# Optimization experiments

Hardware: AMD Instinct MI355X
Metric: run time of the kernel (lower is better)

Reference implementation:

```python
import jax, jax.numpy as jnp
import numpy as np

# hypercfg constants (init_kwargs)
AUX = 0.05
L1W = 5.0
VPW = 1.0
VNW = 1.0


def _lsa_square(cost):
    """Jonker-Volgenant shortest-augmenting-path Hungarian on a square numpy
    cost matrix. Returns rows[j] = row assigned to column j. Runs on host,
    mirroring the original CPU scipy.optimize.linear_sum_assignment call."""
    n = cost.shape[0]
    INF = np.inf
    u = np.zeros(n + 1)
    v = np.zeros(n + 1)
    p = np.zeros(n + 1, dtype=np.int64)   # p[j] = row matched to column j (1-indexed)
    way = np.zeros(n + 1, dtype=np.int64)
    for i in range(1, n + 1):
        p[0] = i
        j0 = 0
        minv = np.full(n + 1, INF)
        used = np.zeros(n + 1, dtype=bool)
        while True:
            used[j0] = True
            i0 = p[j0]
            cur = cost[i0 - 1, :] - u[i0] - v[1:]
            free = ~used[1:]
            upd = free & (cur < minv[1:])
            minv1 = minv[1:]
            minv1[upd] = cur[upd]
            way1 = way[1:]
            way1[upd] = j0
            mfree = np.where(free, minv1, INF)
            j1 = int(np.argmin(mfree)) + 1
            delta = mfree[j1 - 1]
            used_idx = np.nonzero(used)[0]
            u[p[used_idx]] += delta
            v[used_idx] -= delta
            minv1[free] -= delta
            j0 = j1
            if p[j0] == 0:
                break
        while j0 != 0:
            j1 = way[j0]
            p[j0] = p[j1]
            j0 = j1
    return p[1:] - 1


def _match(cost_mk):
    """Rectangular assignment, cost [M, K] with K <= M: pad with a constant
    column block (dummy columns cost the same for any row, so the real K
    columns get the optimal assignment, matching scipy on rectangles)."""
    M, K = cost_mk.shape
    pad = np.zeros((M, M), dtype=np.float64)
    pad[:, :K] = cost_mk
    rows = _lsa_square(pad)
    return rows[:K]


def _cost(meta_points, meta_visibles, gtpoints, gtvisibles):
    # meta_points: [S,B,L,M,2]  gtpoints: [S,B,K,2]
    # meta_visibles: [S,B,M,1]  gtvisibles: [S,B,K,1]
    S, B, L, M, _ = meta_points.shape
    # pairwise L1 cost: [S,B,L,M,K]
    diff = jnp.abs(meta_points[:, :, :, :, None, :] - gtpoints[:, :, None, None, :, :]).sum(-1)
    # delta[l] = L - (l+1), per-layer slack (torch.linspace(1, L, L))
    delta = (L - jnp.arange(1, L + 1, dtype=meta_points.dtype)) * AUX
    cost_p_ml = jax.nn.relu(diff - delta[None, None, :, None, None])
    gtv = gtvisibles[:, :, :, 0][:, :, None, :]          # [S,B,1,K]
    cost_p = gtv * cost_p_ml.mean(2)                     # [S,B,M,K]
    cost_vp = -gtv * jnp.log(meta_visibles)              # [S,B,M,1] -> [S,B,M,K]
    cost_vn = -(1.0 - gtv) * jnp.log(1.0 - meta_visibles)
    cost = L1W * cost_p + VPW * cost_vp + VNW * cost_vn  # [S,B,M,K]
    return cost.mean(0)                                  # mean over shots -> [B,M,K]


def setup_inputs() -> dict:
    key = jax.random.key(0)
    ks = jax.random.split(key, 5)
    S, B, L, M, K = 6, 16, 8, 256, 128
    meta_points = jax.random.uniform(ks[0], (S, B, L, M, 2), dtype=jnp.float32)
    # keep probabilities strictly inside (0,1) so log() is finite
    meta_visibles = jax.random.uniform(ks[1], (S, B, M, 1), dtype=jnp.float32) * 0.9 + 0.05
    covisibles = jax.random.uniform(ks[2], (B, K), dtype=jnp.float32)
    gtpoints = jax.random.uniform(ks[3], (S, B, K, 2), dtype=jnp.float32)
    gtvisibles = (jax.random.uniform(ks[4], (S, B, K, 1)) > 0.5).astype(jnp.float32)
    return {
        "meta_points": meta_points,
        "meta_visibles": meta_visibles,
        "covisibles": covisibles,
        "gtpoints": gtpoints,
        "gtvisibles": gtvisibles,
    }


def reference(meta_points, meta_visibles, covisibles, gtpoints, gtvisibles):
    # covisibles only provides the batch size in the original module
    cost = np.asarray(jax.jit(_cost)(meta_points, meta_visibles, gtpoints, gtvisibles))
    bs = cost.shape[0]
    # per-batch Hungarian on host (sequential data-dependent algorithm);
    # result[b, k] = meta index matched to keypoint k (already kp-sorted,
    # matching the argsort-reorder in the torch code)
    out = np.stack([_match(cost[b]) for b in range(bs)])
    return jnp.asarray(out, dtype=jnp.int64)
```

## Files before the change

### kernel.cpp

```cpp
#include <hip/hip_runtime.h>
#include <math.h>


#define S_ 6
#define B_ 16
#define L_ 8
#define M_ 256
#define K_ 128

__global__ void cost_kernel(const float* __restrict__ mp,
                            const float* __restrict__ mv,
                            const float* __restrict__ gt,
                            const float* __restrict__ gv,
                            float* __restrict__ cost)
{
#pragma clang fp contract(off)
    const int b = blockIdx.x;
    const int m = blockIdx.y;
    const int k = threadIdx.x;

    float accS = 0.0f;
    for (int s = 0; s < S_; ++s) {
        const int sb = s * B_ + b;
        const float gx = gt[(sb * K_ + k) * 2 + 0];
        const float gy = gt[(sb * K_ + k) * 2 + 1];
        float accL = 0.0f;
#pragma unroll
        for (int l = 0; l < L_; ++l) {
            const int base = ((sb * L_ + l) * M_ + m) * 2;
            const float dx = fabsf(mp[base + 0] - gx);
            const float dy = fabsf(mp[base + 1] - gy);
            const float diff = dx + dy;
            const float dl = (float)(L_ - (l + 1)) * 0.05f;
            const float t = diff - dl;
            accL += fmaxf(t, 0.0f);
        }
        const float meanL = accL * 0.125f;
        const float mvv = mv[sb * M_ + m];
        const float gtv = gv[sb * K_ + k];
        const float lp = -logf(mvv);
        const float ln = -logf(1.0f - mvv);
        const float val = (gtv != 0.0f) ? (5.0f * meanL + lp) : ln;
        accS += val;
    }
    cost[(b * M_ + m) * K_ + k] = accS * (1.0f / 6.0f);
}

__device__ __forceinline__ double bits2d(int lo, int hi) {
    const unsigned long long u =
        ((unsigned long long)(unsigned)hi << 32) | (unsigned)lo;
    return __longlong_as_double((long long)u);
}
__device__ __forceinline__ void d2bits(double d, int& lo, int& hi) {
    const unsigned long long u = (unsigned long long)__double_as_longlong(d);
    lo = (int)(u & 0xffffffffull);
    hi = (int)(u >> 32);
}

__global__ __launch_bounds__(64, 1) void match_kernel(const float* __restrict__ cost,
                                                      int* __restrict__ out)
{
#pragma clang fp contract(off)
    const int b = blockIdx.x;
    const int lane = threadIdx.x;
    const float* C = cost + (size_t)b * M_ * K_;
    const double INF = __builtin_inf();
    const int BIG = 0x7fffffff;

    __shared__ float  C_lds[M_ * K_];
    __shared__ double u_lds[257];
    __shared__ int    p_lds[257];

    for (int t = lane; t < (M_ * K_) / 4; t += 64)
        ((float4*)C_lds)[t] = ((const float4*)C)[t];

    for (int t = lane; t < 257; t += 64) {
        u_lds[t] = 0.0;
        p_lds[t] = (t >= 129) ? (t - 128) : 0;
    }
    __syncthreads();

    double v0 = 0.0, v1 = 0.0, v2 = 0.0, v3 = 0.0;

    for (int i = 129; i <= 256; ++i) {
        int used = 0;
        const int pj0 = p_lds[2 * lane + 1];
        const int pj1 = p_lds[2 * lane + 2];
        const int pj2 = p_lds[2 * lane + 129];
        const int pj3 = p_lds[2 * lane + 130];
        double ur0 = u_lds[pj0], ur1 = u_lds[pj1];
        double ur2 = u_lds[pj2], ur3 = u_lds[pj3];
        const double up0 = ur0, up1 = ur1, up2 = ur2, up3 = ur3;

        float2 cc = *(const float2*)(C_lds + (i - 1) * K_ + 2 * lane);
        double u_i0 = 0.0;
        int j1 = 0;
        double usum = 0.0;

        for (;;) {
            double cd0 = ((double)cc.x - u_i0) - v0;
            double cd1 = ((double)cc.y - u_i0) - v1;
            double cd2 = (0.0 - u_i0) - v2;
            double cd3 = (0.0 - u_i0) - v3;
            if (used & 1) cd0 = INF;
            if (used & 2) cd1 = INF;
            if (used & 4) cd2 = INF;
            if (used & 8) cd3 = INF;

            const double m01 = fmin(cd0, cd1);
            const double m23 = fmin(cd2, cd3);
            double bv = fmin(m01, m23);

            int lo, hi; d2bits(bv, lo, hi);
#define MIN_STAGE(CTRL, RM)                                                      \
            {                                                                    \
                const int nlo = __builtin_amdgcn_update_dpp(lo, lo, CTRL, RM, 0xf, false); \
                const int nhi = __builtin_amdgcn_update_dpp(hi, hi, CTRL, RM, 0xf, false); \
                const double mv2 = fmin(bits2d(lo, hi), bits2d(nlo, nhi));       \
                d2bits(mv2, lo, hi);                                             \
            }
            MIN_STAGE(0x111, 0xf)
            MIN_STAGE(0x112, 0xf)
            MIN_STAGE(0x114, 0xf)
            MIN_STAGE(0x118, 0xf)
            MIN_STAGE(0x142, 0xa)
            MIN_STAGE(0x143, 0xc)
#undef MIN_STAGE
            const int mlo = __builtin_amdgcn_readlane(lo, 63);
            const int mhi = __builtin_amdgcn_readlane(hi, 63);
            const double delta = bits2d(mlo, mhi);

            int jr = BIG;
            if (cd1 == delta) jr = 2 * lane + 2;
            if (cd0 == delta) jr = 2 * lane + 1;
            int jd = BIG;
            if (cd3 == delta) jd = 2 * lane + 130;
            if (cd2 == delta) jd = 2 * lane + 129;
            const unsigned long long br = __ballot(jr != BIG);
            const unsigned long long bd = __ballot(jd != BIG);
            const unsigned long long bb = br ? br : bd;
            const int cand = (br != 0ull) ? jr : jd;
            j1 = __builtin_amdgcn_readlane(cand, (int)__builtin_ctzll(bb));

            int ol, sl;
            if (j1 >= 129) { ol = (j1 - 129) >> 1; sl = 2 + ((j1 - 129) & 1); }
            else           { ol = (j1 - 1) >> 1;   sl = (j1 - 1) & 1; }
            const int psel = (sl == 0) ? pj0 : (sl == 1) ? pj1 : (sl == 2) ? pj2 : pj3;
            const int i0n = (j1 >= 129) ? (j1 - 128)
                                        : __builtin_amdgcn_readlane(psel, ol);

            const int rown = (i0n > 0 ? i0n : 1) - 1;
            const float2 ccn = *(const float2*)(C_lds + rown * K_ + 2 * lane);

            usum += delta;
            if (used & 1) { ur0 += delta; v0 -= delta; }
            if (used & 2) { ur1 += delta; v1 -= delta; }
            if (used & 4) { ur2 += delta; v2 -= delta; }
            if (used & 8) { ur3 += delta; v3 -= delta; }

            const double usel = (sl == 0) ? up0 : (sl == 1) ? up1 : (sl == 2) ? up2 : up3;
            int ulo, uhi; d2bits(usel, ulo, uhi);
            const double u_n = bits2d(__builtin_amdgcn_readlane(ulo, ol),
                                      __builtin_amdgcn_readlane(uhi, ol));

            if (i0n == 0) break;

            if (lane == ol) used |= (1 << sl);
            u_i0 = u_n;
            cc = ccn;
        }

        __syncthreads();
        if (used & 1) u_lds[pj0] = ur0;
        if (used & 2) u_lds[pj1] = ur1;
        if (used & 4) u_lds[pj2] = ur2;
        if (used & 8) u_lds[pj3] = ur3;
        if (lane == 0) { p_lds[j1] = i; u_lds[i] = usum; }
        __syncthreads();
    }

    for (int j = lane; j < K_; j += 64)
        out[b * K_ + j] = p_lds[j + 1] - 1;
}

extern "C" void kernel_launch(void* const* d_in, const int* in_sizes, int n_in,
                              void* d_out, int out_size, void* d_ws, size_t ws_size,
                              hipStream_t stream) {
    const float* mp = (const float*)d_in[0];
    const float* mv = (const float*)d_in[1];
    const float* gt = (const float*)d_in[3];
    const float* gv = (const float*)d_in[4];
    int* out = (int*)d_out;
    float* cost = (float*)d_ws;

    dim3 gridA(B_, M_);
    cost_kernel<<<gridA, K_, 0, stream>>>(mp, mv, gt, gv, cost);
    match_kernel<<<B_, 64, 0, stream>>>(cost, out);
}
```

Before: 1.417 ms.

## Handle dummy columns via per-row sorted queue instead of scanning them

Result: slower. 1.558 ms (+9.9%).

```diff
diff --git a/kernel.cpp b/kernel.cpp
--- a/kernel.cpp
+++ b/kernel.cpp
@@ -56,6 +56,13 @@
     lo = (int)(u & 0xffffffffull);
     hi = (int)(u >> 32);
 }
+__device__ __forceinline__ unsigned long long vkey_desc(double v) {
+    const double c = v + 0.0;
+    const unsigned long long bts = (unsigned long long)__double_as_longlong(c);
+    const unsigned long long mask =
+        (unsigned long long)((long long)bts >> 63) | 0x8000000000000000ull;
+    return ~(bts ^ mask);
+}
 
 __global__ __launch_bounds__(64, 1) void match_kernel(const float* __restrict__ cost,
                                                       int* __restrict__ out)
@@ -67,9 +74,13 @@
     const double INF = __builtin_inf();
     const int BIG = 0x7fffffff;
 
-    __shared__ float  C_lds[M_ * K_];
-    __shared__ double u_lds[257];
-    __shared__ int    p_lds[257];
+    __shared__ float   C_lds[M_ * K_];
+    __shared__ double  u_lds[257];
+    __shared__ int     p_lds[257];
+    __shared__ double  vd_lds[128];
+    __shared__ double2 vurec[130];
+    __shared__ int     jrec[130];
+    __shared__ double  Dcons[128];
 
     for (int t = lane; t < (M_ * K_) / 4; t += 64)
         ((float4*)C_lds)[t] = ((const float4*)C)[t];
@@ -78,38 +89,72 @@
         u_lds[t] = 0.0;
         p_lds[t] = (t >= 129) ? (t - 128) : 0;
     }
+    for (int t = lane; t < 128; t += 64) vd_lds[t] = 0.0;
     __syncthreads();
 
-    double v0 = 0.0, v1 = 0.0, v2 = 0.0, v3 = 0.0;
+    double v0 = 0.0, v1 = 0.0;
 
     for (int i = 129; i <= 256; ++i) {
-        int used = 0;
         const int pj0 = p_lds[2 * lane + 1];
         const int pj1 = p_lds[2 * lane + 2];
-        const int pj2 = p_lds[2 * lane + 129];
-        const int pj3 = p_lds[2 * lane + 130];
-        double ur0 = u_lds[pj0], ur1 = u_lds[pj1];
-        double ur2 = u_lds[pj2], ur3 = u_lds[pj3];
-        const double up0 = ur0, up1 = ur1, up2 = ur2, up3 = ur3;
-
         float2 cc = *(const float2*)(C_lds + (i - 1) * K_ + 2 * lane);
+        const double up0 = u_lds[pj0], up1 = u_lds[pj1];
+        double ur0 = up0, ur1 = up1;
+
+        unsigned long long ks0 = vkey_desc(vd_lds[2 * lane]);
+        unsigned long long ks1 = vkey_desc(vd_lds[2 * lane + 1]);
+        int js0 = 2 * lane + 129;
+        int js1 = 2 * lane + 130;
+        for (int k = 2; k <= 128; k <<= 1) {
+            const bool asc = ((lane & (k >> 1)) == 0);
+            for (int d2 = k >> 1; d2 >= 1; d2 >>= 1) {
+                if (d2 == 1) {
+                    const bool L = (ks0 < ks1) || (ks0 == ks1 && js0 < js1);
+                    if (L != asc) {
+                        const unsigned long long tk = ks0; ks0 = ks1; ks1 = tk;
+                        const int tj = js0; js0 = js1; js1 = tj;
+                    }
+                } else {
+                    const int d = d2 >> 1;
+                    const unsigned long long pk0 = __shfl_xor(ks0, d);
+                    const int pj0s = __shfl_xor(js0, d);
+                    const unsigned long long pk1 = __shfl_xor(ks1, d);
+                    const int pj1s = __shfl_xor(js1, d);
+                    const bool lower = ((lane & d) == 0);
+                    const bool L0 = (ks0 < pk0) || (ks0 == pk0 && js0 < pj0s);
+                    const bool L1 = (ks1 < pk1) || (ks1 == pk1 && js1 < pj1s);
+                    const bool keep0 = (lower == asc) ? L0 : !L0;
+                    const bool keep1 = (lower == asc) ? L1 : !L1;
+                    if (!keep0) { ks0 = pk0; js0 = pj0s; }
+                    if (!keep1) { ks1 = pk1; js1 = pj1s; }
+                }
+            }
+        }
+        jrec[2 * lane] = js0;
+        jrec[2 * lane + 1] = js1;
+        vurec[2 * lane]     = make_double2(vd_lds[js0 - 129], u_lds[js0 - 128]);
+        vurec[2 * lane + 1] = make_double2(vd_lds[js1 - 129], u_lds[js1 - 128]);
+        if (lane == 0) { vurec[128] = make_double2(-INF, 0.0); jrec[128] = 257; }
+        __syncthreads();
+
+        double2 vuC = vurec[0]; int jdC = jrec[0];
+        double2 vuN = vurec[1]; int jdN = jrec[1];
+        int ptr = 0;
+
+        int used = 0;
         double u_i0 = 0.0;
+        double usum = 0.0;
         int j1 = 0;
-        double usum = 0.0;
 
         for (;;) {
+            const float2 ccs = *(const float2*)(C_lds + (jdC - 129) * K_ + 2 * lane);
+            const double dval = (0.0 - u_i0) - vuC.x;
+
             double cd0 = ((double)cc.x - u_i0) - v0;
             double cd1 = ((double)cc.y - u_i0) - v1;
-            double cd2 = (0.0 - u_i0) - v2;
-            double cd3 = (0.0 - u_i0) - v3;
             if (used & 1) cd0 = INF;
             if (used & 2) cd1 = INF;
-            if (used & 4) cd2 = INF;
-            if (used & 8) cd3 = INF;
-
-            const double m01 = fmin(cd0, cd1);
-            const double m23 = fmin(cd2, cd3);
-            double bv = fmin(m01, m23);
+            double bv = fmin(cd0, cd1);
 
             int lo, hi; d2bits(bv, lo, hi);
 #define MIN_STAGE(CTRL, RM)                                                      \
@@ -128,53 +173,62 @@
 #undef MIN_STAGE
             const int mlo = __builtin_amdgcn_readlane(lo, 63);
             const int mhi = __builtin_amdgcn_readlane(hi, 63);
-            const double delta = bits2d(mlo, mhi);
-
-            int jr = BIG;
-            if (cd1 == delta) jr = 2 * lane + 2;
-            if (cd0 == delta) jr = 2 * lane + 1;
-            int jd = BIG;
-            if (cd3 == delta) jd = 2 * lane + 130;
-            if (cd2 == delta) jd = 2 * lane + 129;
-            const unsigned long long br = __ballot(jr != BIG);
-            const unsigned long long bd = __ballot(jd != BIG);
-            const unsigned long long bb = br ? br : bd;
-            const int cand = (br != 0ull) ? jr : jd;
-            j1 = __builtin_amdgcn_readlane(cand, (int)__builtin_ctzll(bb));
-
-            int ol, sl;
-            if (j1 >= 129) { ol = (j1 - 129) >> 1; sl = 2 + ((j1 - 129) & 1); }
-            else           { ol = (j1 - 1) >> 1;   sl = (j1 - 1) & 1; }
-            const int psel = (sl == 0) ? pj0 : (sl == 1) ? pj1 : (sl == 2) ? pj2 : pj3;
-            const int i0n = (j1 >= 129) ? (j1 - 128)
-                                        : __builtin_amdgcn_readlane(psel, ol);
-
-            const int rown = (i0n > 0 ? i0n : 1) - 1;
-            const float2 ccn = *(const float2*)(C_lds + rown * K_ + 2 * lane);
-
-            usum += delta;
-            if (used & 1) { ur0 += delta; v0 -= delta; }
-            if (used & 2) { ur1 += delta; v1 -= delta; }
-            if (used & 4) { ur2 += delta; v2 -= delta; }
-            if (used & 8) { ur3 += delta; v3 -= delta; }
-
-            const double usel = (sl == 0) ? up0 : (sl == 1) ? up1 : (sl == 2) ? up2 : up3;
-            int ulo, uhi; d2bits(usel, ulo, uhi);
-            const double u_n = bits2d(__builtin_amdgcn_readlane(ulo, ol),
-                                      __builtin_amdgcn_readlane(uhi, ol));
-
-            if (i0n == 0) break;
-
-            if (lane == ol) used |= (1 << sl);
-            u_i0 = u_n;
-            cc = ccn;
+            const double rmin = bits2d(mlo, mhi);
+
+            if (rmin <= dval) {
+                const double delta = rmin;
+                usum += delta;
+                if (used & 1) { ur0 += delta; v0 -= delta; }
+                if (used & 2) { ur1 += delta; v1 -= delta; }
+
+                int jr = BIG;
+                if (cd1 == delta) jr = 2 * lane + 2;
+                if (cd0 == delta) jr = 2 * lane + 1;
+                const unsigned long long br = __ballot(jr != BIG);
+                j1 = __builtin_amdgcn_readlane(jr, (int)__builtin_ctzll(br));
+
+                const int ol = (j1 - 1) >> 1, sl = (j1 - 1) & 1;
+                const int psel = sl ? pj1 : pj0;
+                const int i0n = __builtin_amdgcn_readlane(psel, ol);
+                if (i0n == 0) break;
+
+                const double usel = sl ? up1 : up0;
+                int ulo, uhi; d2bits(usel, ulo, uhi);
+                const double u_n = bits2d(__builtin_amdgcn_readlane(ulo, ol),
+                                          __builtin_amdgcn_readlane(uhi, ol));
+                if (lane == ol) used |= (1 << sl);
+                u_i0 = u_n;
+                cc = *(const float2*)(C_lds + (i0n - 1) * K_ + 2 * lane);
+            } else {
+                const double delta = dval;
+                usum += delta;
+                if (used & 1) { ur0 += delta; v0 -= delta; }
+                if (used & 2) { ur1 += delta; v1 -= delta; }
+                if (lane == 0) Dcons[ptr] = usum;
+                u_i0 = vuC.y;
+                cc = ccs;
+                vuC = vuN; jdC = jdN;
+                ++ptr;
+                vuN = vurec[ptr + 1]; jdN = jrec[ptr + 1];
+            }
         }
 
         __syncthreads();
         if (used & 1) u_lds[pj0] = ur0;
         if (used & 2) u_lds[pj1] = ur1;
-        if (used & 4) u_lds[pj2] = ur2;
-        if (used & 8) u_lds[pj3] = ur3;
+        {
+            const int t0i = 2 * lane, t1i = 2 * lane + 1;
+            if (t0i < ptr) {
+                const double amt = usum - Dcons[t0i];
+                u_lds[js0 - 128] += amt;
+                vd_lds[js0 - 129] -= amt;
+            }
+            if (t1i < ptr) {
+                const double amt = usum - Dcons[t1i];
+                u_lds[js1 - 128] += amt;
+                vd_lds[js1 - 129] -= amt;
+            }
+        }
         if (lane == 0) { p_lds[j1] = i; u_lds[i] = usum; }
         __syncthreads();
     }
```

## Track dummy-column minimum via precomputed max-v candidate in Hungarian loop

Applied to the files above, without the earlier changes.

Result: slower. 1.485 ms (+4.8%).

```diff
diff --git a/kernel.cpp b/kernel.cpp
--- a/kernel.cpp
+++ b/kernel.cpp
@@ -56,6 +56,26 @@
     lo = (int)(u & 0xffffffffull);
     hi = (int)(u >> 32);
 }
+__device__ __forceinline__ double readlane_d(double d, int l) {
+    int lo, hi; d2bits(d, lo, hi);
+    return bits2d(__builtin_amdgcn_readlane(lo, l),
+                  __builtin_amdgcn_readlane(hi, l));
+}
+
+#define RSTG(LOV, HIV, FOP, CTRL, RM)                                            \
+    {                                                                            \
+        const int nlo_ = __builtin_amdgcn_update_dpp(LOV, LOV, CTRL, RM, 0xf, false); \
+        const int nhi_ = __builtin_amdgcn_update_dpp(HIV, HIV, CTRL, RM, 0xf, false); \
+        const double r_ = FOP(bits2d(LOV, HIV), bits2d(nlo_, nhi_));             \
+        d2bits(r_, LOV, HIV);                                                    \
+    }
+#define RLADDER(LOV, HIV, FOP)                                                   \
+    RSTG(LOV, HIV, FOP, 0x111, 0xf)                              \
+    RSTG(LOV, HIV, FOP, 0x112, 0xf)                              \
+    RSTG(LOV, HIV, FOP, 0x114, 0xf)                              \
+    RSTG(LOV, HIV, FOP, 0x118, 0xf)                              \
+    RSTG(LOV, HIV, FOP, 0x142, 0xa)                \
+    RSTG(LOV, HIV, FOP, 0x143, 0xc)
 
 __global__ __launch_bounds__(64, 1) void match_kernel(const float* __restrict__ cost,
                                                       int* __restrict__ out)
@@ -65,6 +85,7 @@
     const int lane = threadIdx.x;
     const float* C = cost + (size_t)b * M_ * K_;
     const double INF = __builtin_inf();
+    const double NINF = -__builtin_inf();
     const int BIG = 0x7fffffff;
 
     __shared__ float  C_lds[M_ * K_];
@@ -81,101 +102,120 @@
     __syncthreads();
 
     double v0 = 0.0, v1 = 0.0, v2 = 0.0, v3 = 0.0;
+    const int jd2 = 2 * lane + 129;
+    const int jd3 = 2 * lane + 130;
+
+    int jdC = 129; double vdC = 0.0, udC = 0.0;
 
     for (int i = 129; i <= 256; ++i) {
-        int used = 0;
         const int pj0 = p_lds[2 * lane + 1];
         const int pj1 = p_lds[2 * lane + 2];
-        const int pj2 = p_lds[2 * lane + 129];
-        const int pj3 = p_lds[2 * lane + 130];
         double ur0 = u_lds[pj0], ur1 = u_lds[pj1];
-        double ur2 = u_lds[pj2], ur3 = u_lds[pj3];
+        double ur2 = u_lds[2 * lane + 1], ur3 = u_lds[2 * lane + 2];
         const double up0 = ur0, up1 = ur1, up2 = ur2, up3 = ur3;
 
         float2 cc = *(const float2*)(C_lds + (i - 1) * K_ + 2 * lane);
         double u_i0 = 0.0;
+        int used = 0;
         int j1 = 0;
         double usum = 0.0;
 
         for (;;) {
+            const float2 ccs = *(const float2*)(C_lds + (jdC - 129) * K_ + 2 * lane);
+            const double dval = (0.0 - u_i0) - vdC;
+
             double cd0 = ((double)cc.x - u_i0) - v0;
             double cd1 = ((double)cc.y - u_i0) - v1;
-            double cd2 = (0.0 - u_i0) - v2;
-            double cd3 = (0.0 - u_i0) - v3;
             if (used & 1) cd0 = INF;
             if (used & 2) cd1 = INF;
-            if (used & 4) cd2 = INF;
-            if (used & 8) cd3 = INF;
-
-            const double m01 = fmin(cd0, cd1);
-            const double m23 = fmin(cd2, cd3);
-            double bv = fmin(m01, m23);
+            double bv = fmin(cd0, cd1);
 
             int lo, hi; d2bits(bv, lo, hi);
-#define MIN_STAGE(CTRL, RM)                                                      \
-            {                                                                    \
-                const int nlo = __builtin_amdgcn_update_dpp(lo, lo, CTRL, RM, 0xf, false); \
-                const int nhi = __builtin_amdgcn_update_dpp(hi, hi, CTRL, RM, 0xf, false); \
-                const double mv2 = fmin(bits2d(lo, hi), bits2d(nlo, nhi));       \
-                d2bits(mv2, lo, hi);                                             \
-            }
-            MIN_STAGE(0x111, 0xf)
-            MIN_STAGE(0x112, 0xf)
-            MIN_STAGE(0x114, 0xf)
-            MIN_STAGE(0x118, 0xf)
-            MIN_STAGE(0x142, 0xa)
-            MIN_STAGE(0x143, 0xc)
-#undef MIN_STAGE
+            RLADDER(lo, hi, fmin)
             const int mlo = __builtin_amdgcn_readlane(lo, 63);
             const int mhi = __builtin_amdgcn_readlane(hi, 63);
-            const double delta = bits2d(mlo, mhi);
-
-            int jr = BIG;
-            if (cd1 == delta) jr = 2 * lane + 2;
-            if (cd0 == delta) jr = 2 * lane + 1;
-            int jd = BIG;
-            if (cd3 == delta) jd = 2 * lane + 130;
-            if (cd2 == delta) jd = 2 * lane + 129;
-            const unsigned long long br = __ballot(jr != BIG);
-            const unsigned long long bd = __ballot(jd != BIG);
-            const unsigned long long bb = br ? br : bd;
-            const int cand = (br != 0ull) ? jr : jd;
-            j1 = __builtin_amdgcn_readlane(cand, (int)__builtin_ctzll(bb));
-
-            int ol, sl;
-            if (j1 >= 129) { ol = (j1 - 129) >> 1; sl = 2 + ((j1 - 129) & 1); }
-            else           { ol = (j1 - 1) >> 1;   sl = (j1 - 1) & 1; }
-            const int psel = (sl == 0) ? pj0 : (sl == 1) ? pj1 : (sl == 2) ? pj2 : pj3;
-            const int i0n = (j1 >= 129) ? (j1 - 128)
-                                        : __builtin_amdgcn_readlane(psel, ol);
-
-            const int rown = (i0n > 0 ? i0n : 1) - 1;
-            const float2 ccn = *(const float2*)(C_lds + rown * K_ + 2 * lane);
-
-            usum += delta;
-            if (used & 1) { ur0 += delta; v0 -= delta; }
-            if (used & 2) { ur1 += delta; v1 -= delta; }
-            if (used & 4) { ur2 += delta; v2 -= delta; }
-            if (used & 8) { ur3 += delta; v3 -= delta; }
-
-            const double usel = (sl == 0) ? up0 : (sl == 1) ? up1 : (sl == 2) ? up2 : up3;
-            int ulo, uhi; d2bits(usel, ulo, uhi);
-            const double u_n = bits2d(__builtin_amdgcn_readlane(ulo, ol),
-                                      __builtin_amdgcn_readlane(uhi, ol));
-
-            if (i0n == 0) break;
-
-            if (lane == ol) used |= (1 << sl);
-            u_i0 = u_n;
-            cc = ccn;
+            const double rmin = bits2d(mlo, mhi);
+
+            const double vm2 = ((used & 4) || (jd2 == jdC)) ? NINF : v2;
+            const double vm3 = ((used & 8) || (jd3 == jdC)) ? NINF : v3;
+            double bx = fmax(vm2, vm3);
+            int xlo, xhi; d2bits(bx, xlo, xhi);
+            RLADDER(xlo, xhi, fmax)
+            const double vdN = bits2d(__builtin_amdgcn_readlane(xlo, 63),
+                                      __builtin_amdgcn_readlane(xhi, 63));
+            int jc = BIG;
+            if (vm3 == vdN) jc = jd3;
+            if (vm2 == vdN) jc = jd2;
+            const unsigned long long bd = __ballot(jc != BIG);
+            const int jdN = __builtin_amdgcn_readlane(jc, (int)__builtin_ctzll(bd));
+            const int olN = (jdN - 129) >> 1, slN = (jdN - 129) & 1;
+            const double udN = readlane_d(slN ? up3 : up2, olN);
+
+            if (rmin <= dval) {
+                const double delta = rmin;
+                int jr = BIG;
+                if (cd1 == delta) jr = 2 * lane + 2;
+                if (cd0 == delta) jr = 2 * lane + 1;
+                const unsigned long long br = __ballot(jr != BIG);
+                j1 = __builtin_amdgcn_readlane(jr, (int)__builtin_ctzll(br));
+
+                const int ol = (j1 - 1) >> 1, sl = (j1 - 1) & 1;
+                const int psel = sl ? pj1 : pj0;
+                const int i0n = __builtin_amdgcn_readlane(psel, ol);
+
+                const int rown = (i0n > 0 ? i0n : 1) - 1;
+                const float2 ccn = *(const float2*)(C_lds + rown * K_ + 2 * lane);
+
+                usum += delta;
+                if (used & 1) { ur0 += delta; v0 -= delta; }
+                if (used & 2) { ur1 += delta; v1 -= delta; }
+                if (used & 4) { ur2 += delta; v2 -= delta; }
+                if (used & 8) { ur3 += delta; v3 -= delta; }
+
+                const double u_n = readlane_d(sl ? up1 : up0, ol);
+
+                if (i0n == 0) break;
+                if (lane == ol) used |= (1 << sl);
+                u_i0 = u_n;
+                cc = ccn;
+            } else {
+                const double delta = dval;
+                usum += delta;
+                if (used & 1) { ur0 += delta; v0 -= delta; }
+                if (used & 2) { ur1 += delta; v1 -= delta; }
+                if (used & 4) { ur2 += delta; v2 -= delta; }
+                if (used & 8) { ur3 += delta; v3 -= delta; }
+
+                j1 = jdC;
+                const int olc = (jdC - 129) >> 1, slc = (jdC - 129) & 1;
+                if (lane == olc) used |= (4 << slc);
+                u_i0 = udC;
+                cc = ccs;
+                jdC = jdN; vdC = vdN; udC = udN;
+            }
         }
 
         __syncthreads();
         if (used & 1) u_lds[pj0] = ur0;
         if (used & 2) u_lds[pj1] = ur1;
-        if (used & 4) u_lds[pj2] = ur2;
-        if (used & 8) u_lds[pj3] = ur3;
+        if (used & 4) u_lds[2 * lane + 1] = ur2;
+        if (used & 8) u_lds[2 * lane + 2] = ur3;
         if (lane == 0) { p_lds[j1] = i; u_lds[i] = usum; }
+
+        {
+            double bx = fmax(v2, v3);
+            int xlo, xhi; d2bits(bx, xlo, xhi);
+            RLADDER(xlo, xhi, fmax)
+            vdC = bits2d(__builtin_amdgcn_readlane(xlo, 63),
+                         __builtin_amdgcn_readlane(xhi, 63));
+            int jc = BIG;
+            if (v3 == vdC) jc = jd3;
+            if (v2 == vdC) jc = jd2;
+            const unsigned long long bd = __ballot(jc != BIG);
+            jdC = __builtin_amdgcn_readlane(jc, (int)__builtin_ctzll(bd));
+            const int olc = (jdC - 129) >> 1, slc = (jdC - 129) & 1;
+            udC = readlane_d(slc ? ur3 : ur2, olc);
+        }
         __syncthreads();
     }
 
```
